# Performance work log

Measured on AMD Instinct MI355X. Metric: run time of the kernel, lower is better.

Reference implementation:

```python
import jax, jax.numpy as jnp
import numpy as np
import math

B, L = 64, 285          # L=285 hard-coded in source (expand(-1, 285, -1))
ITEM_DIM, POS_DIM = 128, 128
DIM = ITEM_DIM + POS_DIM
N_ITEMS, N_POS = 100000, 300
W_SCALE = 20.0
N_ITER = 50             # entmax_bisect default iterations


def _pfn(z, am1):
    # p = clamp(z, 0) ** (1/(alpha-1))
    return jnp.maximum(z, 0.0) ** (1.0 / am1)


def entmax_bisect(X, alpha):
    """alpha-entmax over the LAST axis via bisection (Peters & Martins).
    alpha broadcasts against X (e.g. [B,L,1] or [B,1,1] vs [B,L,L])."""
    d = X.shape[-1]
    am1 = alpha - 1.0
    Xs = X * am1
    max_val = jnp.max(Xs, axis=-1, keepdims=True)
    tau_lo = max_val - 1.0                      # gp(1, alpha) = 1
    tau_hi = max_val - (1.0 / d) ** am1         # gp(1/d, alpha)
    f_lo = jnp.sum(_pfn(Xs - tau_lo, am1), -1, keepdims=True) - 1.0
    dm0 = tau_hi - tau_lo

    def body(i, carry):
        tau_lo, dm, p = carry
        dm = dm * 0.5
        tau_m = tau_lo + dm
        p = _pfn(Xs - tau_m, am1)
        f_m = jnp.sum(p, -1, keepdims=True) - 1.0
        tau_lo = jnp.where(f_m * f_lo >= 0, tau_m, tau_lo)
        return tau_lo, dm, p

    _, _, p = jax.lax.fori_loop(0, N_ITER, body, (tau_lo, dm0, jnp.zeros_like(Xs)))
    return p / jnp.sum(p, -1, keepdims=True)


def layer_norm(x, g, b, eps=1e-5):
    m = jnp.mean(x, -1, keepdims=True)
    v = jnp.var(x, -1, keepdims=True)
    return (x - m) * jax.lax.rsqrt(v + eps) * g + b


def _add_value(a):
    return jnp.where(a == 1.0, 1.0001, a)


def setup_inputs() -> dict:
    key = jax.random.key(0)
    ks = jax.random.split(key, 16)
    emb_w = 0.1 * jax.random.normal(ks[2], (N_ITEMS + 1, ITEM_DIM), jnp.float32)
    emb_w = emb_w.at[0].set(0.0)            # padding_idx=0
    pos_emb_w = 0.1 * jax.random.normal(ks[3], (N_POS, POS_DIM), jnp.float32)
    pos_emb_w = pos_emb_w.at[0].set(0.0)
    return {
        "x": jax.random.randint(ks[0], (B, L), 0, N_ITEMS, dtype=jnp.int32),
        "pos": jax.random.randint(ks[1], (B, L), 0, N_POS, dtype=jnp.int32),
        "emb_w": emb_w,
        "pos_emb_w": pos_emb_w,
        "atten_w0": 0.05 * jax.random.normal(ks[4], (1, DIM), jnp.float32),
        "atten_w1": 0.05 * jax.random.normal(ks[5], (DIM, DIM), jnp.float32),
        "atten_w2": 0.05 * jax.random.normal(ks[6], (DIM, DIM), jnp.float32),
        "atten_bias": jnp.zeros((DIM,), jnp.float32),
        "mlp_w": 0.05 * jax.random.normal(ks[7], (DIM, DIM), jnp.float32),
        "mlp_b": jnp.zeros((DIM,), jnp.float32),
        "sa_w1_w": 0.05 * jax.random.normal(ks[8], (DIM, DIM), jnp.float32),
        "sa_w1_b": jnp.zeros((DIM,), jnp.float32),
        "sa_w2_w": 0.05 * jax.random.normal(ks[9], (DIM, DIM), jnp.float32),
        "sa_w2_b": jnp.zeros((DIM,), jnp.float32),
        "ln_g": jnp.ones((DIM,), jnp.float32),
        "ln_b": jnp.zeros((DIM,), jnp.float32),
        "w_f_w": 0.05 * jax.random.normal(ks[10], (ITEM_DIM, 2 * DIM), jnp.float32),
        "w_f_b": jnp.zeros((ITEM_DIM,), jnp.float32),
        "alpha_w_w": 0.05 * jax.random.normal(ks[11], (1, DIM), jnp.float32),
        "alpha_w_b": jnp.zeros((1,), jnp.float32),
    }


def reference(x, pos, emb_w, pos_emb_w, atten_w0, atten_w1, atten_w2, atten_bias,
              mlp_w, mlp_b, sa_w1_w, sa_w1_b, sa_w2_w, sa_w2_b, ln_g, ln_b,
              w_f_w, w_f_b, alpha_w_w, alpha_w_b):
    neg_inf = jnp.float32(-jnp.inf)
    x_emb = emb_w[x]                                    # [B,L,item_dim]
    p_emb = pos_emb_w[pos]                              # [B,L,pos_dim]
    mask = (x != 0).astype(jnp.float32)                 # [B,L]
    x_ = jnp.concatenate([x_emb, p_emb], axis=-1)       # [B,L,DIM]
    x_s = x_[:, :-1, :]                                 # [B,L-1,DIM]

    # entmax alpha for self-attention (broadcasts like the [B,285,1] expand)
    a_ent = _add_value(jax.nn.sigmoid(x_[:, -1, :] @ alpha_w_w.T + alpha_w_b) + 1.0)
    a_ent = a_ent[:, None, :]                           # [B,1,1]

    # ---- self attention ----
    q_ = jax.nn.relu(x_ @ mlp_w.T + mlp_b)
    scores = jnp.einsum('bqd,bkd->bqk', q_, x_) / math.sqrt(DIM)
    scores = jnp.where(mask[:, None, :] == 0, neg_inf, scores)
    att = entmax_bisect(scores, a_ent)                  # [B,L,L]
    att_v = jnp.einsum('bqk,bkd->bqd', att, x_)
    att_v = (jax.nn.relu(att_v @ sa_w1_w.T + sa_w1_b) @ sa_w2_w.T + sa_w2_b) + att_v
    att_v = layer_norm(att_v, ln_g, ln_b)
    m_s = att_v[:, -1:, :]                              # [B,1,DIM]
    x_n = att_v[:, :-1, :]                              # [B,L-1,DIM]

    # ---- global attention ----
    a_glob = _add_value(jax.nn.sigmoid(m_s @ alpha_w_w.T + alpha_w_b) + 1.0)  # [B,1,1]
    al = jax.nn.relu(x_n @ atten_w1 + m_s @ atten_w2 + atten_bias) @ atten_w0.T  # [B,L-1,1]
    al = jnp.where(mask[:, :-1, None] == 0, neg_inf, al)
    # entmax over dim=1: move it to last axis
    aw = entmax_bisect(al.transpose(0, 2, 1), a_glob)   # [B,1,L-1]
    global_c = jnp.einsum('bok,bkd->bod', aw, x_s)      # [B,1,DIM]

    # ---- decoder ----
    c = jax.nn.selu(jnp.concatenate([global_c, m_s], -1) @ w_f_w.T + w_f_b)  # [B,1,item_dim]
    c = c[:, 0, :]
    l_c = c / jnp.linalg.norm(c, axis=-1, keepdims=True)
    l_emb = emb_w[1:-1]
    l_emb = l_emb / jnp.linalg.norm(l_emb, axis=-1, keepdims=True)
    z = W_SCALE * (l_c @ l_emb.T)                       # [B, N_ITEMS-1]
    return z
```

## Files before the change

kernel.cpp:

```cpp
#include <hip/hip_runtime.h>
#include <hip/hip_bf16.h>
#include <math.h>

#define LQ 285
#define LD_S 288
#define ENT_ITERS 30
#define NOUT 99999
#define LDK 72
#define LDZ 136

typedef __attribute__((ext_vector_type(8))) short bf16x8;
typedef __attribute__((ext_vector_type(4))) float f32x4;

__device__ __forceinline__ float wsum(float v){
  #pragma unroll
  for (int o=32;o;o>>=1) v += __shfl_xor(v,o);
  return v;
}
__device__ __forceinline__ float wmax(float v){
  #pragma unroll
  for (int o=32;o;o>>=1) v = fmaxf(v, __shfl_xor(v,o));
  return v;
}
__device__ __forceinline__ float pfn(float z, float inv){
  return z > 0.f ? __builtin_amdgcn_exp2f(inv * __builtin_amdgcn_logf(z)) : 0.f;
}
__device__ __forceinline__ short f2bf(float f){
  __hip_bfloat16 h = __float2bfloat16(f);
  return *(short*)&h;
}

__global__ __launch_bounds__(256) void k_gather(const int* __restrict__ x, const int* __restrict__ pos,
    const float* __restrict__ emb, const float* __restrict__ pemb,
    float* __restrict__ xo, short* __restrict__ xbf){
  int bl = blockIdx.x;
  int d  = threadIdx.x;
  int xi = x[bl], pi = pos[bl];
  float v = (d < 128) ? emb[(size_t)xi*128 + d] : pemb[(size_t)pi*128 + (d-128)];
  xo [(size_t)bl*256 + d] = v;
  xbf[(size_t)bl*256 + d] = f2bf(v);
}

__global__ __launch_bounds__(256) void k_castw(const float* __restrict__ w0, const float* __restrict__ w1,
    const float* __restrict__ w2, const float* __restrict__ w3, short* __restrict__ dst){
  int idx = blockIdx.x*256 + threadIdx.x;
  int which = idx >> 16, off = idx & 65535;
  const float* s = which==0 ? w0 : which==1 ? w1 : which==2 ? w2 : w3;
  dst[idx] = f2bf(s[off]);
}

__global__ __launch_bounds__(64) void k_aent(const float* __restrict__ x_, const float* __restrict__ aw,
    const float* __restrict__ ab, float* __restrict__ a_ent){
  int b = blockIdx.x, lane = threadIdx.x;
  const float* r = x_ + ((size_t)b*LQ + (LQ-1))*256;
  float s = 0.f;
  #pragma unroll
  for (int j=0;j<4;++j){ int k = lane + j*64; s = fmaf(r[k], aw[k], s); }
  s = wsum(s);
  if (lane==0){
    float a = 1.f/(1.f + expf(-(s + ab[0]))) + 1.f;
    if (a == 1.f) a = 1.0001f;
    a_ent[b] = a;
  }
}

template<bool BT, int EPI, bool OF32, bool OBF>
__global__ __launch_bounds__(256) void k_mgemm(
    const short* __restrict__ A, int lda, long long strA, int kpadA,
    const short* __restrict__ Bm, int ldb, long long strB,
    float* __restrict__ C, short* __restrict__ Cbf, int ldc, long long strC,
    int M, int N, int K,
    const float* __restrict__ bias,
    const float* __restrict__ res,
    const int* __restrict__ xids,
    float scale)
{
  __shared__ __align__(16) short As[64*LDK];
  __shared__ __align__(16) short Bs[64*LDK];
  const int bz = blockIdx.z;
  A  += (size_t)bz * strA;
  Bm += (size_t)bz * strB;
  if (OF32) C   += (size_t)bz * strC;
  if (OBF)  Cbf += (size_t)bz * strC;
  const int* xb = xids ? xids + (size_t)bz*LQ : nullptr;
  const int t  = threadIdx.x;
  const int wv = t >> 6, ln = t & 63;
  const int l16 = ln & 15, kseg = ln >> 4;
  const int m0 = blockIdx.y*64, n0 = blockIdx.x*64;

  f32x4 acc[4] = {};

  for (int k0 = 0; k0 < K; k0 += 64){
    #pragma unroll
    for (int it=0; it<2; ++it){
      int idx8 = t + it*256;
      int r = idx8 >> 3, c8 = (idx8 & 7) << 3;
      int gr = m0 + r, gk = k0 + c8;
      bf16x8 v = {};
      if (gr < M){
        if (gk + 8 <= kpadA){
          v = *(const bf16x8*)(A + (size_t)gr*lda + gk);
        } else {
          #pragma unroll
          for (int e=0;e<8;++e) if (gk+e < K) v[e] = A[(size_t)gr*lda + gk+e];
        }
      }
      *(bf16x8*)&As[r*LDK + c8] = v;
    }
    if (BT){
      #pragma unroll
      for (int it=0; it<2; ++it){
        int idx8 = t + it*256;
        int n = idx8 >> 3, c8 = (idx8 & 7) << 3;
        int gn = n0 + n, gk = k0 + c8;
        bf16x8 v = {};
        if (gn < N){
          if (gk + 8 <= K){
            v = *(const bf16x8*)(Bm + (size_t)gn*ldb + gk);
          } else {
            #pragma unroll
            for (int e=0;e<8;++e) if (gk+e < K) v[e] = Bm[(size_t)gn*ldb + gk+e];
          }
        }
        *(bf16x8*)&Bs[n*LDK + c8] = v;
      }
    } else {
      #pragma unroll
      for (int j=0; j<8; ++j){
        int idx2 = t + j*256;
        int kk = idx2 >> 5, n2 = (idx2 & 31) << 1;
        int gk = k0 + kk;
        short lo = 0, hi = 0;
        if (gk < K){
          int vv = *(const int*)(Bm + (size_t)gk*ldb + n0 + n2);
          lo = (short)(vv & 0xffff); hi = (short)((unsigned)vv >> 16);
        }
        Bs[(n2  )*LDK + kk] = lo;
        Bs[(n2+1)*LDK + kk] = hi;
      }
    }
    __syncthreads();
    #pragma unroll
    for (int ks=0; ks<64; ks+=32){
      bf16x8 af = *(const bf16x8*)&As[(wv*16 + l16)*LDK + ks + kseg*8];
      #pragma unroll
      for (int ct=0; ct<4; ++ct){
        bf16x8 bf = *(const bf16x8*)&Bs[(ct*16 + l16)*LDK + ks + kseg*8];
        acc[ct] = __builtin_amdgcn_mfma_f32_16x16x32_bf16(af, bf, acc[ct], 0, 0, 0);
      }
    }
    __syncthreads();
  }
  #pragma unroll
  for (int ct=0; ct<4; ++ct){
    int col = n0 + ct*16 + l16;
    if (col >= N) continue;
    #pragma unroll
    for (int i=0;i<4;++i){
      int row = m0 + wv*16 + kseg*4 + i;
      if (row >= M) continue;
      float v = acc[ct][i];
      if (EPI == 1)      v = fmaxf(v + bias[col], 0.f);
      else if (EPI == 2) v = v + bias[col] + res[(size_t)row*ldc + col];
      else if (EPI == 3){ v *= scale; if (xb[col] == 0) v = -INFINITY; }
      else if (EPI == 4) v = fmaxf(v + bias[(row/LQ)*256 + col], 0.f);
      if (OF32) C  [(size_t)row*ldc + col] = v;
      if (OBF)  Cbf[(size_t)row*ldc + col] = f2bf(v);
    }
  }
}

__global__ __launch_bounds__(256) void k_entmax1(const float* __restrict__ att, const float* __restrict__ a_ent,
    short* __restrict__ attbf){
  int wid = blockIdx.x*4 + (threadIdx.x >> 6);
  int lane = threadIdx.x & 63;
  int b = wid / LQ;
  const float* row = att + (size_t)wid * LD_S;
  short* orow = attbf + (size_t)wid * LD_S;
  float alpha = a_ent[b], am1 = alpha - 1.f, inv = 1.f/am1;
  float Xs[5];
  #pragma unroll
  for (int j=0;j<5;++j){ int k = lane + j*64; Xs[j] = (k < LQ) ? row[k]*am1 : -INFINITY; }
  float mx = Xs[0];
  #pragma unroll
  for (int j=1;j<5;++j) mx = fmaxf(mx, Xs[j]);
  mx = wmax(mx);
  float tau_lo = mx - 1.f;
  float tau_hi = mx - __builtin_amdgcn_exp2f(am1 * __builtin_amdgcn_logf(1.f/(float)LQ));
  float s = 0.f;
  #pragma unroll
  for (int j=0;j<5;++j) s += pfn(Xs[j]-tau_lo, inv);
  float f_lo = wsum(s) - 1.f;
  float dm = tau_hi - tau_lo;
  float p[5]; float fsum = 1.f;
  for (int it=0; it<ENT_ITERS; ++it){
    dm *= 0.5f;
    float tau = tau_lo + dm;
    float sl = 0.f;
    #pragma unroll
    for (int j=0;j<5;++j){ float pj = pfn(Xs[j]-tau, inv); p[j]=pj; sl += pj; }
    fsum = wsum(sl);
    if ((fsum - 1.f)*f_lo >= 0.f) tau_lo = tau;
  }
  float rs = 1.f/fsum;
  #pragma unroll
  for (int j=0;j<5;++j){
    int k = lane + j*64;
    if (k < LQ) orow[k] = f2bf(p[j]*rs);
    else if (k < LD_S) orow[k] = 0;
  }
}

__global__ __launch_bounds__(256) void k_ln(float* __restrict__ v2, const float* __restrict__ g,
    const float* __restrict__ bb, short* __restrict__ obf){
  __shared__ float red[4];
  int r = blockIdx.x, t = threadIdx.x;
  float v = v2[(size_t)r*256 + t];
  float s = wsum(v);
  if ((t&63)==0) red[t>>6] = s;
  __syncthreads();
  float mean = (red[0]+red[1]+red[2]+red[3]) * (1.f/256.f);
  __syncthreads();
  float d = v - mean;
  float ss = wsum(d*d);
  if ((t&63)==0) red[t>>6] = ss;
  __syncthreads();
  float var = (red[0]+red[1]+red[2]+red[3]) * (1.f/256.f);
  float o = d * rsqrtf(var + 1e-5f) * g[t] + bb[t];
  v2[(size_t)r*256 + t] = o;
  obf[(size_t)r*256 + t] = f2bf(o);
}

__global__ __launch_bounds__(256) void k_msw2(const float* __restrict__ ln, const float* __restrict__ w2,
    const float* __restrict__ abias, const float* __restrict__ aw, const float* __restrict__ ab,
    float* __restrict__ msw2, float* __restrict__ a_glob){
  __shared__ float ms[256];
  __shared__ float red[4];
  int b = blockIdx.x, t = threadIdx.x;
  float m = ln[((size_t)b*LQ + (LQ-1))*256 + t];
  ms[t] = m;
  float s = wsum(m * aw[t]);
  if ((t&63)==0) red[t>>6] = s;
  __syncthreads();
  if (t == 0){
    float dot = red[0]+red[1]+red[2]+red[3] + ab[0];
    float a = 1.f/(1.f + expf(-dot)) + 1.f;
    if (a == 1.f) a = 1.0001f;
    a_glob[b] = a;
  }
  float acc = abias[t];
  for (int d=0; d<256; ++d) acc = fmaf(ms[d], w2[d*256 + t], acc);
  msw2[b*256 + t] = acc;
}

__global__ __launch_bounds__(256) void k_al(const float* __restrict__ tbuf, const float* __restrict__ w0,
    const int* __restrict__ x, float* __restrict__ al){
  int wid = blockIdx.x*4 + (threadIdx.x >> 6);
  int lane = threadIdx.x & 63;
  int b = wid / 284, r = wid % 284;
  const float* tr = tbuf + ((size_t)b*LQ + r)*256;
  float s = 0.f;
  #pragma unroll
  for (int j=0;j<4;++j){ int k = lane + j*64; s = fmaf(tr[k], w0[k], s); }
  s = wsum(s);
  if (lane == 0) al[b*284 + r] = (x[b*LQ + r] != 0) ? s : -INFINITY;
}

__global__ __launch_bounds__(256) void k_second(
    const float* __restrict__ al, const float* __restrict__ a_glob,
    const float* __restrict__ x_, const float* __restrict__ ln,
    const float* __restrict__ wfw, const float* __restrict__ wfb,
    short* __restrict__ lcbf){
  __shared__ float red[4];
  __shared__ float saw[284];
  __shared__ float gcs[256];
  __shared__ float ms[256];
  __shared__ float cb[128];
  int b = blockIdx.x, t = threadIdx.x;
  int wv = t >> 6, lane = t & 63;
  if (wv == 0){
    float alpha = a_glob[b], am1 = alpha - 1.f, inv = 1.f/am1;
    float Xs[5];
    #pragma unroll
    for (int j=0;j<5;++j){ int k = lane + j*64; Xs[j] = (k < 284) ? al[b*284 + k]*am1 : -INFINITY; }
    float mx = Xs[0];
    #pragma unroll
    for (int j=1;j<5;++j) mx = fmaxf(mx, Xs[j]);
    mx = wmax(mx);
    float tau_lo = mx - 1.f;
    float tau_hi = mx - __builtin_amdgcn_exp2f(am1 * __builtin_amdgcn_logf(1.f/284.f));
    float s = 0.f;
    #pragma unroll
    for (int j=0;j<5;++j) s += pfn(Xs[j]-tau_lo, inv);
    float f_lo = wsum(s) - 1.f;
    float dm = tau_hi - tau_lo;
    float p[5]; float fsum = 1.f;
    for (int it=0; it<ENT_ITERS; ++it){
      dm *= 0.5f;
      float tau = tau_lo + dm;
      float sl = 0.f;
      #pragma unroll
      for (int j=0;j<5;++j){ float pj = pfn(Xs[j]-tau, inv); p[j]=pj; sl += pj; }
      fsum = wsum(sl);
      if ((fsum - 1.f)*f_lo >= 0.f) tau_lo = tau;
    }
    float rs = 1.f/fsum;
    #pragma unroll
    for (int j=0;j<5;++j){ int k = lane + j*64; if (k < 284) saw[k] = p[j]*rs; }
  }
  __syncthreads();
  float g = 0.f;
  for (int k=0; k<284; ++k) g = fmaf(saw[k], x_[((size_t)b*LQ + k)*256 + t], g);
  gcs[t] = g;
  ms[t]  = ln[((size_t)b*LQ + (LQ-1))*256 + t];
  __syncthreads();
  if (t < 128){
    float acc = wfb[t];
    const float* wr = wfw + (size_t)t*512;
    for (int d=0; d<256; ++d) acc = fmaf(gcs[d], wr[d], acc);
    for (int d=0; d<256; ++d) acc = fmaf(ms[d], wr[256+d], acc);
    const float SC = 1.0507009873554805f, AL = 1.6732632423543772f;
    acc = acc > 0.f ? SC*acc : SC*AL*(expf(acc) - 1.f);
    cb[t] = acc;
  }
  __syncthreads();
  float sq = (t < 128) ? cb[t]*cb[t] : 0.f;
  sq = wsum(sq);
  if ((t&63)==0) red[t>>6] = sq;
  __syncthreads();
  float nrm = rsqrtf(red[0]+red[1]+red[2]+red[3]);
  if (t < 128) lcbf[b*128 + t] = f2bf(cb[t]*nrm);
}

__global__ __launch_bounds__(256) void k_z2(const float* __restrict__ emb, const short* __restrict__ lcbf,
    float* __restrict__ z){
  __shared__ __align__(16) short Ls[64*LDZ];
  __shared__ __align__(16) short Es[64*LDZ];
  int t = threadIdx.x;
  int i0 = blockIdx.x*64;
  int r = t >> 2, q = t & 3;
  {
    const short* src = lcbf + r*128 + q*32;
    #pragma unroll
    for (int u=0;u<4;++u)
      *(bf16x8*)&Ls[r*LDZ + q*32 + u*8] = *(const bf16x8*)(src + u*8);
  }
  {
    int gi = i0 + r;
    const float* er = emb + ((size_t)gi+1)*128 + q*32;
    float4 v[8];
    float ss = 0.f;
    #pragma unroll
    for (int u=0;u<8;++u){
      float4 x4 = (gi < NOUT) ? ((const float4*)er)[u] : make_float4(0.f,0.f,0.f,0.f);
      v[u] = x4;
      ss = fmaf(x4.x,x4.x, fmaf(x4.y,x4.y, fmaf(x4.z,x4.z, fmaf(x4.w,x4.w, ss))));
    }
    ss += __shfl_xor(ss,1);
    ss += __shfl_xor(ss,2);
    float inv = rsqrtf(ss);
    short sh[32];
    #pragma unroll
    for (int u=0;u<8;++u){
      sh[u*4+0] = f2bf(v[u].x*inv); sh[u*4+1] = f2bf(v[u].y*inv);
      sh[u*4+2] = f2bf(v[u].z*inv); sh[u*4+3] = f2bf(v[u].w*inv);
    }
    #pragma unroll
    for (int u=0;u<4;++u)
      *(bf16x8*)&Es[r*LDZ + q*32 + u*8] = *(const bf16x8*)&sh[u*8];
  }
  __syncthreads();
  int wv = t >> 6, ln = t & 63, l16 = ln & 15, kseg = ln >> 4;
  f32x4 acc[4] = {};
  #pragma unroll
  for (int ks=0; ks<128; ks+=32){
    bf16x8 af = *(const bf16x8*)&Ls[(wv*16 + l16)*LDZ + ks + kseg*8];
    #pragma unroll
    for (int ct=0; ct<4; ++ct){
      bf16x8 bfr = *(const bf16x8*)&Es[(ct*16 + l16)*LDZ + ks + kseg*8];
      acc[ct] = __builtin_amdgcn_mfma_f32_16x16x32_bf16(af, bfr, acc[ct], 0, 0, 0);
    }
  }
  #pragma unroll
  for (int ct=0; ct<4; ++ct){
    int col = i0 + ct*16 + l16;
    if (col >= NOUT) continue;
    #pragma unroll
    for (int i=0;i<4;++i){
      int row = wv*16 + kseg*4 + i;
      z[(size_t)row*NOUT + col] = 20.f * acc[ct][i];
    }
  }
}

extern "C" void kernel_launch(void* const* d_in, const int* in_sizes, int n_in,
                              void* d_out, int out_size, void* d_ws, size_t ws_size,
                              hipStream_t stream){
  const int*   x          = (const int*)d_in[0];
  const int*   pos        = (const int*)d_in[1];
  const float* emb_w      = (const float*)d_in[2];
  const float* pos_emb_w  = (const float*)d_in[3];
  const float* atten_w0   = (const float*)d_in[4];
  const float* atten_w1   = (const float*)d_in[5];
  const float* atten_w2   = (const float*)d_in[6];
  const float* atten_bias = (const float*)d_in[7];
  const float* mlp_w      = (const float*)d_in[8];
  const float* mlp_b      = (const float*)d_in[9];
  const float* sa_w1_w    = (const float*)d_in[10];
  const float* sa_w1_b    = (const float*)d_in[11];
  const float* sa_w2_w    = (const float*)d_in[12];
  const float* sa_w2_b    = (const float*)d_in[13];
  const float* ln_g       = (const float*)d_in[14];
  const float* ln_b       = (const float*)d_in[15];
  const float* w_f_w      = (const float*)d_in[16];
  const float* w_f_b      = (const float*)d_in[17];
  const float* alpha_w_w  = (const float*)d_in[18];
  const float* alpha_w_b  = (const float*)d_in[19];
  float* z = (float*)d_out;

  float* ws = (float*)d_ws;
  const size_t NX = (size_t)64*LQ*256;
  const size_t NS = (size_t)64*LQ*LD_S;
  float* x_    = ws;
  float* bq    = ws + NX;
  float* sc    = ws + 2*NX;
  float* attv  = ws + 2*NX + NS;
  float* v2    = sc;
  float* lnb   = v2;
  float* small = ws + 3*NX + NS;
  float* a_ent  = small;
  float* a_glob = small + 64;
  float* msw2   = small + 128;
  float* albuf  = small + 128 + 16384;
  short* bfbase = (short*)(ws + 3*NX + NS + 43008);
  short* x_bf   = bfbase;
  short* gbf    = bfbase + NX;
  short* attbf  = bfbase + 2*NX;
  short* attvbf = attbf + NS;
  short* lnbf   = attvbf + NX;
  short* wbf    = lnbf + NX;
  short* w_mlp  = wbf;
  short* w_sa1  = wbf + 65536;
  short* w_sa2  = wbf + 2*65536;
  short* w_aw1  = wbf + 3*65536;
  short* lcbf   = wbf + 4*65536;

  k_gather<<<18240, 256, 0, stream>>>(x, pos, emb_w, pos_emb_w, x_, x_bf);
  k_castw<<<1024, 256, 0, stream>>>(mlp_w, sa_w1_w, sa_w2_w, atten_w1, wbf);
  k_aent<<<64, 64, 0, stream>>>(x_, alpha_w_w, alpha_w_b, a_ent);
  k_mgemm<true,1,false,true><<<dim3(4,285,1), 256, 0, stream>>>(
      x_bf,256,0,256, w_mlp,256,0, nullptr, gbf,256,0,
      18240,256,256, mlp_b, nullptr, nullptr, 0.f);
  k_mgemm<true,3,true,false><<<dim3(5,5,64), 256, 0, stream>>>(
      gbf,256,(long long)LQ*256,256, x_bf,256,(long long)LQ*256,
      sc, nullptr, LD_S,(long long)LQ*LD_S,
      285,285,256, nullptr, nullptr, x, 0.0625f);
  k_entmax1<<<4560, 256, 0, stream>>>(sc, a_ent, attbf);
  k_mgemm<false,0,true,true><<<dim3(4,5,64), 256, 0, stream>>>(
      attbf,LD_S,(long long)LQ*LD_S,LD_S, x_bf,256,(long long)LQ*256,
      attv, attvbf, 256,(long long)LQ*256,
      285,256,285, nullptr, nullptr, nullptr, 0.f);
  k_mgemm<true,1,false,true><<<dim3(4,285,1), 256, 0, stream>>>(
      attvbf,256,0,256, w_sa1,256,0, nullptr, gbf,256,0,
      18240,256,256, sa_w1_b, nullptr, nullptr, 0.f);
  k_mgemm<true,2,true,false><<<dim3(4,285,1), 256, 0, stream>>>(
      gbf,256,0,256, w_sa2,256,0, v2, nullptr, 256,0,
      18240,256,256, sa_w2_b, attv, nullptr, 0.f);
  k_ln<<<18240, 256, 0, stream>>>(v2, ln_g, ln_b, lnbf);
  k_msw2<<<64, 256, 0, stream>>>(lnb, atten_w2, atten_bias, alpha_w_w, alpha_w_b, msw2, a_glob);
  k_mgemm<false,4,true,false><<<dim3(4,285,1), 256, 0, stream>>>(
      lnbf,256,0,256, w_aw1,256,0, bq, nullptr, 256,0,
      18240,256,256, msw2, nullptr, nullptr, 0.f);
  k_al<<<4544, 256, 0, stream>>>(bq, atten_w0, x, albuf);
  k_second<<<64, 256, 0, stream>>>(albuf, a_glob, x_, lnb, w_f_w, w_f_b, lcbf);
  k_z2<<<1563, 256, 0, stream>>>(emb_w, lcbf, z);
}
```

Before: 411.0 us.

## Use 128-row tiles in flattened GEMMs and trim entmax bisection iterations

```diff
diff --git a/kernel.cpp b/kernel.cpp
--- a/kernel.cpp
+++ b/kernel.cpp
@@ -4,7 +4,7 @@
 
 #define LQ 285
 #define LD_S 288
-#define ENT_ITERS 30
+#define ENT_ITERS 26
 #define NOUT 99999
 #define LDK 72
 #define LDZ 136
@@ -64,7 +64,7 @@
   }
 }
 
-template<bool BT, int EPI, bool OF32, bool OBF>
+template<int BM, bool BT, int EPI, bool OF32, bool OBF>
 __global__ __launch_bounds__(256) void k_mgemm(
     const short* __restrict__ A, int lda, long long strA, int kpadA,
     const short* __restrict__ Bm, int ldb, long long strB,
@@ -75,7 +75,8 @@
     const int* __restrict__ xids,
     float scale)
 {
-  __shared__ __align__(16) short As[64*LDK];
+  constexpr int MR = BM/64;
+  __shared__ __align__(16) short As[BM*LDK];
   __shared__ __align__(16) short Bs[64*LDK];
   const int bz = blockIdx.z;
   A  += (size_t)bz * strA;
@@ -86,13 +87,13 @@
   const int t  = threadIdx.x;
   const int wv = t >> 6, ln = t & 63;
   const int l16 = ln & 15, kseg = ln >> 4;
-  const int m0 = blockIdx.y*64, n0 = blockIdx.x*64;
-
-  f32x4 acc[4] = {};
+  const int m0 = blockIdx.y*BM, n0 = blockIdx.x*64;
+
+  f32x4 acc[MR][4] = {};
 
   for (int k0 = 0; k0 < K; k0 += 64){
     #pragma unroll
-    for (int it=0; it<2; ++it){
+    for (int it=0; it<BM/32; ++it){
       int idx8 = t + it*256;
       int r = idx8 >> 3, c8 = (idx8 & 7) << 3;
       int gr = m0 + r, gk = k0 + c8;
@@ -142,30 +143,38 @@
     __syncthreads();
     #pragma unroll
     for (int ks=0; ks<64; ks+=32){
-      bf16x8 af = *(const bf16x8*)&As[(wv*16 + l16)*LDK + ks + kseg*8];
-      #pragma unroll
-      for (int ct=0; ct<4; ++ct){
-        bf16x8 bf = *(const bf16x8*)&Bs[(ct*16 + l16)*LDK + ks + kseg*8];
-        acc[ct] = __builtin_amdgcn_mfma_f32_16x16x32_bf16(af, bf, acc[ct], 0, 0, 0);
+      bf16x8 bfr[4];
+      #pragma unroll
+      for (int ct=0; ct<4; ++ct)
+        bfr[ct] = *(const bf16x8*)&Bs[(ct*16 + l16)*LDK + ks + kseg*8];
+      #pragma unroll
+      for (int mr=0; mr<MR; ++mr){
+        bf16x8 af = *(const bf16x8*)&As[(wv*16*MR + mr*16 + l16)*LDK + ks + kseg*8];
+        #pragma unroll
+        for (int ct=0; ct<4; ++ct)
+          acc[mr][ct] = __builtin_amdgcn_mfma_f32_16x16x32_bf16(af, bfr[ct], acc[mr][ct], 0, 0, 0);
       }
     }
     __syncthreads();
   }
   #pragma unroll
-  for (int ct=0; ct<4; ++ct){
-    int col = n0 + ct*16 + l16;
-    if (col >= N) continue;
-    #pragma unroll
-    for (int i=0;i<4;++i){
-      int row = m0 + wv*16 + kseg*4 + i;
-      if (row >= M) continue;
-      float v = acc[ct][i];
-      if (EPI == 1)      v = fmaxf(v + bias[col], 0.f);
-      else if (EPI == 2) v = v + bias[col] + res[(size_t)row*ldc + col];
-      else if (EPI == 3){ v *= scale; if (xb[col] == 0) v = -INFINITY; }
-      else if (EPI == 4) v = fmaxf(v + bias[(row/LQ)*256 + col], 0.f);
-      if (OF32) C  [(size_t)row*ldc + col] = v;
-      if (OBF)  Cbf[(size_t)row*ldc + col] = f2bf(v);
+  for (int mr=0; mr<MR; ++mr){
+    #pragma unroll
+    for (int ct=0; ct<4; ++ct){
+      int col = n0 + ct*16 + l16;
+      if (col >= N) continue;
+      #pragma unroll
+      for (int i=0;i<4;++i){
+        int row = m0 + wv*16*MR + mr*16 + kseg*4 + i;
+        if (row >= M) continue;
+        float v = acc[mr][ct][i];
+        if (EPI == 1)      v = fmaxf(v + bias[col], 0.f);
+        else if (EPI == 2) v = v + bias[col] + res[(size_t)row*ldc + col];
+        else if (EPI == 3){ v *= scale; if (xb[col] == 0) v = -INFINITY; }
+        else if (EPI == 4) v = fmaxf(v + bias[(row/LQ)*256 + col], 0.f);
+        if (OF32) C  [(size_t)row*ldc + col] = v;
+        if (OBF)  Cbf[(size_t)row*ldc + col] = f2bf(v);
+      }
     }
   }
 }
@@ -448,27 +457,27 @@
   k_gather<<<18240, 256, 0, stream>>>(x, pos, emb_w, pos_emb_w, x_, x_bf);
   k_castw<<<1024, 256, 0, stream>>>(mlp_w, sa_w1_w, sa_w2_w, atten_w1, wbf);
   k_aent<<<64, 64, 0, stream>>>(x_, alpha_w_w, alpha_w_b, a_ent);
-  k_mgemm<true,1,false,true><<<dim3(4,285,1), 256, 0, stream>>>(
+  k_mgemm<128,true,1,false,true><<<dim3(4,143,1), 256, 0, stream>>>(
       x_bf,256,0,256, w_mlp,256,0, nullptr, gbf,256,0,
       18240,256,256, mlp_b, nullptr, nullptr, 0.f);
-  k_mgemm<true,3,true,false><<<dim3(5,5,64), 256, 0, stream>>>(
+  k_mgemm<64,true,3,true,false><<<dim3(5,5,64), 256, 0, stream>>>(
       gbf,256,(long long)LQ*256,256, x_bf,256,(long long)LQ*256,
       sc, nullptr, LD_S,(long long)LQ*LD_S,
       285,285,256, nullptr, nullptr, x, 0.0625f);
   k_entmax1<<<4560, 256, 0, stream>>>(sc, a_ent, attbf);
-  k_mgemm<false,0,true,true><<<dim3(4,5,64), 256, 0, stream>>>(
+  k_mgemm<64,false,0,true,true><<<dim3(4,5,64), 256, 0, stream>>>(
       attbf,LD_S,(long long)LQ*LD_S,LD_S, x_bf,256,(long long)LQ*256,
       attv, attvbf, 256,(long long)LQ*256,
       285,256,285, nullptr, nullptr, nullptr, 0.f);
-  k_mgemm<true,1,false,true><<<dim3(4,285,1), 256, 0, stream>>>(
+  k_mgemm<128,true,1,false,true><<<dim3(4,143,1), 256, 0, stream>>>(
       attvbf,256,0,256, w_sa1,256,0, nullptr, gbf,256,0,
       18240,256,256, sa_w1_b, nullptr, nullptr, 0.f);
-  k_mgemm<true,2,true,false><<<dim3(4,285,1), 256, 0, stream>>>(
+  k_mgemm<128,true,2,true,false><<<dim3(4,143,1), 256, 0, stream>>>(
       gbf,256,0,256, w_sa2,256,0, v2, nullptr, 256,0,
       18240,256,256, sa_w2_b, attv, nullptr, 0.f);
   k_ln<<<18240, 256, 0, stream>>>(v2, ln_g, ln_b, lnbf);
   k_msw2<<<64, 256, 0, stream>>>(lnb, atten_w2, atten_bias, alpha_w_w, alpha_w_b, msw2, a_glob);
-  k_mgemm<false,4,true,false><<<dim3(4,285,1), 256, 0, stream>>>(
+  k_mgemm<128,false,4,true,false><<<dim3(4,143,1), 256, 0, stream>>>(
       lnbf,256,0,256, w_aw1,256,0, bq, nullptr, 256,0,
       18240,256,256, msw2, nullptr, nullptr, 0.f);
   k_al<<<4544, 256, 0, stream>>>(bq, atten_w0, x, albuf);
```

After: 415.0 us. Within noise of the previous version (+1.0%).
